# Performance work log

Measured on AMD Instinct MI355X. Metric: run time of the kernel, lower is better.

The kernel has to match this reference:

```python
import jax, jax.numpy as jnp
import numpy as np
from jax import lax

B, C, SD = 2, 64, 512
DW = 2 * C   # DW_Expand=2
FFN = 2 * C  # FFN_Expand=2
D = H = W = 64
K = 3


def _ln3d(x, w, b, eps=1e-6):
    # torch LayerNorm3d: mean/std over channel dim, std is unbiased (ddof=1)
    m = jnp.mean(x, axis=1, keepdims=True)
    s = jnp.std(x, axis=1, keepdims=True, ddof=1)
    return w * ((x - m) / (s + eps)) + b


def _pw(x, w, b):
    # 1x1x1 conv: w [O, I], x [B, I, D, H, W]
    return jnp.einsum('oi,bidhw->bodhw', w, x) + b[None, :, None, None, None]


def setup_inputs() -> dict:
    key = jax.random.key(0)
    ks = jax.random.split(key, 24)
    n = lambda i, shp, sc=1.0: (jax.random.normal(ks[i], shp, jnp.float32) * sc)
    return {
        'inp': n(0, (B, C, D, H, W)),
        'style_vector': n(1, (B, SD)),
        'w1': n(2, (DW, C), 0.1), 'b1': n(3, (DW,), 0.1),
        'mod_w': n(4, (DW, 1, K, K, K), 0.1), 'mod_b': n(5, (DW,), 0.1),
        'style_w': n(6, (DW, SD), 0.05), 'style_b': jnp.ones((DW,), jnp.float32),
        'sca_w': n(7, (DW, DW), 0.1), 'sca_b': n(8, (DW,), 0.1),
        'w3': n(9, (C, DW), 0.1), 'b3': n(10, (C,), 0.1),
        'w4': n(11, (FFN, C), 0.1), 'b4': n(12, (FFN,), 0.1),
        'w5': n(13, (C, FFN), 0.1), 'b5': n(14, (C,), 0.1),
        'ln1_w': jnp.ones((1, C, 1, 1, 1), jnp.float32), 'ln1_b': jnp.zeros((1, C, 1, 1, 1), jnp.float32),
        'ln2_w': jnp.ones((1, C, 1, 1, 1), jnp.float32), 'ln2_b': jnp.zeros((1, C, 1, 1, 1), jnp.float32),
        'beta': n(15, (1, C, 1, 1, 1), 0.1), 'gamma': n(16, (1, C, 1, 1, 1), 0.1),
    }


def _mod_dwconv(x, style, mod_w, mod_b, style_w, style_b):
    # StyleGAN-style per-sample modulated DEPTHWISE 3x3x3 conv.
    # For a depthwise conv, modulating weight per (sample, channel) and
    # demodulating is equivalent to one shared depthwise conv followed by a
    # per-(sample, channel) output scale s*demod.
    s = style @ style_w.T + style_b                      # [B, DW]
    k2 = jnp.sum(mod_w * mod_w, axis=(1, 2, 3, 4))       # [DW]
    demod = lax.rsqrt(k2[None, :] * (s * s) + 1e-8)      # [B, DW]
    y = lax.conv_general_dilated(
        x, mod_w, window_strides=(1, 1, 1), padding=((1, 1), (1, 1), (1, 1)),
        dimension_numbers=('NCDHW', 'OIDHW', 'NCDHW'), feature_group_count=DW)
    return y * (s * demod)[:, :, None, None, None] + mod_b[None, :, None, None, None]


def reference(inp, style_vector, w1, b1, mod_w, mod_b, style_w, style_b,
              sca_w, sca_b, w3, b3, w4, b4, w5, b5,
              ln1_w, ln1_b, ln2_w, ln2_b, beta, gamma):
    x = _ln3d(inp, ln1_w, ln1_b)
    x = _pw(x, w1, b1)
    x = _mod_dwconv(x, style_vector, mod_w, mod_b, style_w, style_b)
    x = jax.nn.gelu(x, approximate=False)
    pooled = jnp.mean(x, axis=(2, 3, 4), keepdims=True)          # [B, DW, 1,1,1]
    gate = jnp.einsum('oi,bicde->bocde', sca_w, pooled) + sca_b[None, :, None, None, None]
    x = x * gate
    x = _pw(x, w3, b3)
    y = inp + x * beta
    x = _pw(_ln3d(y, ln2_w, ln2_b), w4, b4)
    x = jax.nn.gelu(x, approximate=False)
    x = _pw(x, w5, b5)
    return y + x * gamma
```

## Files before the change

### kernel.cpp

```cpp
#include <hip/hip_runtime.h>
#include <hip/hip_bf16.h>

typedef __hip_bfloat16 bf16;
typedef short  sv4 __attribute__((ext_vector_type(4)));
typedef short  sv8 __attribute__((ext_vector_type(8)));
typedef float  f32x4 __attribute__((ext_vector_type(4)));
typedef float  fv2  __attribute__((ext_vector_type(2)));
typedef unsigned int uv4 __attribute__((ext_vector_type(4)));

#define CH      64
#define DWC     128
#define SDIM    512
#define SPATIAL (64*64*64)
#define NB      2
#define NVOX    (NB*SPATIAL)

#define ROWS      65
#define PLANE_CH  (64*ROWS)
#define BG_CH     (64*PLANE_CH)
#define HPAD_CHUNKS ((size_t)32*BG_CH + 16)
#define HPAD_BYTES  (HPAD_CHUNKS*16)

#define OFF_SMOD   0
#define OFF_POOLED 256
#define OFF_PB1    512
#define OFF_PB4    768
#define OFF_PB35   1024
#define OFF_MODWT  1536
#define OFF_U16    5120
#define U16_W1F 0
#define U16_W3F 8192
#define U16_W4F 24576
#define U16_W5F 32768

#define A_BYTES ((size_t)NB * DWC * SPATIAL * 2)

__device__ __forceinline__ float b2f(short u) {
    return __uint_as_float(((unsigned)(unsigned short)u) << 16);
}
__device__ __forceinline__ short f2bs(float f) {
    __hip_bfloat16 h = __float2bfloat16(f);
    return __builtin_bit_cast(short, h);
}
__device__ __forceinline__ float gelu_f(float x) {
    float x2 = x * x;
    float z  = x * fmaf(x2, 0.07135481627f, 1.5957691216f);
    float e  = exp2f(-1.4426950409f * z);
    return x * __builtin_amdgcn_rcpf(1.f + e);
}

__global__ void prep_kernel(const float* __restrict__ style,
                            const float* __restrict__ w1, const float* __restrict__ b1,
                            const float* __restrict__ mod_w,
                            const float* __restrict__ style_w, const float* __restrict__ style_b,
                            const float* __restrict__ b3,
                            const float* __restrict__ w4, const float* __restrict__ b4,
                            const float* __restrict__ w5, const float* __restrict__ b5,
                            const float* __restrict__ ln1w, const float* __restrict__ ln1b,
                            const float* __restrict__ ln2w, const float* __restrict__ ln2b,
                            const float* __restrict__ beta, const float* __restrict__ gamma,
                            float* __restrict__ wsf, sv8* __restrict__ h) {
    int t = threadIdx.x;
    int B = blockIdx.x;
    short* w16 = (short*)(wsf + OFF_U16);

    if (B == 0) {
        if (t < 16) {
            const sv8 zz = {0,0,0,0,0,0,0,0};
            h[(size_t)32*BG_CH + t] = zz;
        }
        if (t < DWC) {
            float bb1 = b1[t], bb4 = b4[t];
            for (int c = 0; c < CH; ++c) {
                bb1 = fmaf(w1[t*CH + c], ln1b[c], bb1);
                bb4 = fmaf(w4[t*CH + c], ln2b[c], bb4);
            }
            wsf[OFF_PB1 + t] = bb1;
            wsf[OFF_PB4 + t] = bb4;
        }
        if (t < CH) {
            wsf[OFF_PB35 + 4*t + 0] = b3[t];
            wsf[OFF_PB35 + 4*t + 1] = beta[t];
            wsf[OFF_PB35 + 4*t + 2] = gamma[t];
            wsf[OFF_PB35 + 4*t + 3] = b5[t];
        }
        for (int idx = t; idx < 27*DWC; idx += 256) {
            int k = idx >> 7, c = idx & 127;
            wsf[OFF_MODWT + idx] = mod_w[c*27 + k];
        }
    }
    {
        int o   = B*32 + (t >> 3);
        int sub = t & 7;
        int b = o >> 7, ch = o & 127;
        const float4* s4 = (const float4*)(style + b*SDIM) + sub*16;
        const float4* wv = (const float4*)(style_w + ch*SDIM) + sub*16;
        float s0=0.f, s1=0.f, s2=0.f, s3=0.f;
        #pragma unroll
        for (int i = 0; i < 16; ++i) {
            float4 a_ = s4[i], b_ = wv[i];
            s0 = fmaf(a_.x, b_.x, s0); s1 = fmaf(a_.y, b_.y, s1);
            s2 = fmaf(a_.z, b_.z, s2); s3 = fmaf(a_.w, b_.w, s3);
        }
        float ps = (s0 + s1) + (s2 + s3);
        ps += __shfl_xor(ps, 1); ps += __shfl_xor(ps, 2); ps += __shfl_xor(ps, 4);
        if (sub == 0) {
            float s = style_b[ch] + ps;
            float k2 = 0.f;
            for (int j = 0; j < 27; ++j) { float w = mod_w[ch*27 + j]; k2 = fmaf(w, w, k2); }
            wsf[OFF_SMOD + o]   = s * rsqrtf(fmaf(k2, s*s, 1e-8f));
            wsf[OFF_POOLED + o] = 0.f;
        }
    }
    for (int idx = B*1024 + t; idx < B*1024 + 1024; idx += 256) {
        int m = idx >> 6, k = idx & 63;
        int dst = (((k >> 3)*DWC + m) << 3) + (k & 7);
        w16[U16_W1F + dst] = f2bs(w1[idx] * ln1w[k]);
        w16[U16_W4F + dst] = f2bs(w4[idx] * ln2w[k]);
    }
    for (int idx = B*1024 + t; idx < B*1024 + 1024; idx += 256) {
        int m = idx >> 7, k = idx & 127;
        w16[U16_W5F + (((k >> 3)*CH + m) << 3) + (k & 7)] = f2bs(w5[idx]);
    }
}

__global__ __launch_bounds__(256) void lnpw1_kernel(const float* __restrict__ inp,
                                                    const float* __restrict__ wsf,
                                                    sv8* __restrict__ h) {
    __shared__ sv8  w1s[1024];
    __shared__ short ht[4*2176];
    int tid  = threadIdx.x;
    int blk  = blockIdx.x;
    int wid  = tid >> 6;
    int lane = tid & 63;
    int col  = lane & 15, grp = lane >> 4;
    int b    = blk >> 12;
    int row  = blk & 4095;
    int vx   = (row << 6) + (wid << 4) + col;

    const float* b1p = wsf + OFF_PB1;
    short* hw = ht + wid*2176;

    const float* xp = inp + (size_t)b * CH * SPATIAL + vx;
    float xv[16];
    #pragma unroll
    for (int e = 0; e < 16; ++e) {
        int k = ((e >> 3) << 5) + (grp << 3) + (e & 7);
        xv[e] = xp[(size_t)k * SPATIAL];
    }
    {
        const sv8* src = (const sv8*)((const short*)(wsf + OFF_U16) + U16_W1F);
        #pragma unroll
        for (int i = 0; i < 4; ++i) w1s[i*256 + tid] = src[i*256 + tid];
    }
    __syncthreads();

    float sum = 0.f, ssq = 0.f;
    #pragma unroll
    for (int e = 0; e < 16; ++e) { sum += xv[e]; ssq = fmaf(xv[e], xv[e], ssq); }
    sum += __shfl_xor(sum, 16); sum += __shfl_xor(sum, 32);
    ssq += __shfl_xor(ssq, 16); ssq += __shfl_xor(ssq, 32);
    float m   = sum * (1.f/64.f);
    float var = fmaxf((ssq - 64.f*m*m) * (1.f/63.f), 0.f);
    float inv = 1.f / (sqrtf(var) + 1e-6f);

    sv8 xb0, xb1;
    #pragma unroll
    for (int i = 0; i < 8; ++i) {
        xb0[i] = f2bs((xv[i]     - m) * inv);
        xb1[i] = f2bs((xv[8 + i] - m) * inv);
    }

    f32x4 acc[8] = {};
    #pragma unroll
    for (int mt = 0; mt < 8; ++mt) {
        acc[mt] = __builtin_amdgcn_mfma_f32_16x16x32_bf16(w1s[(grp    )*DWC + mt*16 + col], xb0, acc[mt], 0, 0, 0);
        acc[mt] = __builtin_amdgcn_mfma_f32_16x16x32_bf16(w1s[(grp + 4)*DWC + mt*16 + col], xb1, acc[mt], 0, 0, 0);
    }

    #pragma unroll
    for (int mt = 0; mt < 8; ++mt) {
        sv4 p;
        #pragma unroll
        for (int r = 0; r < 4; ++r) {
            int f = mt*16 + 4*grp + r;
            p[r] = f2bs(acc[mt][r] + b1p[f]);
        }
        *(sv4*)(hw + col*136 + mt*16 + 4*grp) = p;
    }
    #pragma unroll
    for (int gq = 0; gq < 4; ++gq) {
        int g = gq*4 + grp;
        sv8 vrow = *(const sv8*)(hw + col*136 + g*8);
        size_t base = (size_t)(b*16 + g) * BG_CH + row*ROWS;
        h[base + 1 + (wid << 4) + col] = vrow;
        if (wid == 0 && col == 0) {
            const sv8 zz = {0,0,0,0,0,0,0,0};
            h[base] = zz;
        }
    }
}

__global__ __launch_bounds__(256) void conv_kernel(const sv8* __restrict__ h,
                                                   const float* __restrict__ mod_b,
                                                   const float* __restrict__ wsf,
                                                   sv8* __restrict__ a,
                                                   float* __restrict__ pooled) {
    __shared__ float part[4][8];
    int tid = threadIdx.x;
    int w   = tid & 63;
    int dq  = tid >> 6;
    int hy  = blockIdx.x & 63;
    int bg  = blockIdx.x >> 6;
    int g   = bg & 15;
    int b   = bg >> 4;

    const sv8* hP  = h + (size_t)bg * BG_CH;
    sv8*      adst = a + (size_t)bg * SPATIAL;
    const float* mwt = wsf + OFF_MODWT + g*8;
    const float* smp = wsf + OFF_SMOD + b*DWC + g*8;
    const float* mbp = mod_b + g*8;

    bool r0ok = (hy > 0), r2ok = (hy < 63);
    int d0 = dq << 4;

    fv2 an[4] = {}, am[4] = {}, ao[4] = {};
    fv2 psum[4] = {};

    #pragma unroll 1
    for (int i = 0; i < 18; ++i) {
        int dd = d0 - 1 + i;
        fv2 f[9][4];
        if ((unsigned)dd < 64u) {
            const sv8* p = hP + dd*PLANE_CH + hy*ROWS + 1 + w;
            sv8 cv[9];
            const sv8 zz = {0,0,0,0,0,0,0,0};
            if (r0ok) { cv[0] = p[-ROWS-1]; cv[1] = p[-ROWS]; cv[2] = p[-ROWS+1]; }
            else      { cv[0] = zz; cv[1] = zz; cv[2] = zz; }
            cv[3] = p[-1]; cv[4] = p[0]; cv[5] = p[1];
            if (r2ok) { cv[6] = p[ROWS-1]; cv[7] = p[ROWS]; cv[8] = p[ROWS+1]; }
            else      { cv[6] = zz; cv[7] = zz; cv[8] = zz; }
            #pragma unroll
            for (int r = 0; r < 9; ++r) {
                uv4 u = __builtin_bit_cast(uv4, cv[r]);
                #pragma unroll
                for (int c4 = 0; c4 < 4; ++c4) {
                    fv2 fr;
                    fr.x = __uint_as_float(u[c4] << 16);
                    fr.y = __uint_as_float(u[c4] & 0xFFFF0000u);
                    f[r][c4] = fr;
                }
            }
        } else {
            #pragma unroll
            for (int r = 0; r < 9; ++r)
                #pragma unroll
                for (int c4 = 0; c4 < 4; ++c4) f[r][c4] = (fv2)(0.f);
        }

        if (i >= 2) {
            #pragma unroll
            for (int r = 0; r < 9; ++r) {
                const fv2* wr = (const fv2*)(mwt + (18 + r)*DWC);
                #pragma unroll
                for (int c4 = 0; c4 < 4; ++c4) ao[c4] = wr[c4]*f[r][c4] + ao[c4];
            }
            int o = d0 + i - 2;
            sv8 ov;
            #pragma unroll
            for (int c4 = 0; c4 < 4; ++c4) {
                float v0 = gelu_f(fmaf(ao[c4].x, smp[2*c4],     mbp[2*c4]));
                float v1 = gelu_f(fmaf(ao[c4].y, smp[2*c4 + 1], mbp[2*c4 + 1]));
                psum[c4].x += v0; psum[c4].y += v1;
                ov[2*c4]     = f2bs(v0);
                ov[2*c4 + 1] = f2bs(v1);
            }
            adst[o*4096 + hy*64 + w] = ov;
        }
        if (i >= 1 && i <= 16) {
            #pragma unroll
            for (int r = 0; r < 9; ++r) {
                const fv2* wr = (const fv2*)(mwt + (9 + r)*DWC);
                #pragma unroll
                for (int c4 = 0; c4 < 4; ++c4) am[c4] = wr[c4]*f[r][c4] + am[c4];
            }
        }
        if (i <= 15) {
            #pragma unroll
            for (int c4 = 0; c4 < 4; ++c4) an[c4] = (fv2)(0.f);
            #pragma unroll
            for (int r = 0; r < 9; ++r) {
                const fv2* wr = (const fv2*)(mwt + r*DWC);
                #pragma unroll
                for (int c4 = 0; c4 < 4; ++c4) an[c4] = wr[c4]*f[r][c4] + an[c4];
            }
        }
        #pragma unroll
        for (int c4 = 0; c4 < 4; ++c4) { ao[c4] = am[c4]; am[c4] = an[c4]; }
    }

    #pragma unroll
    for (int c = 0; c < 8; ++c) {
        float s = (c & 1) ? psum[c >> 1].y : psum[c >> 1].x;
        #pragma unroll
        for (int off = 32; off > 0; off >>= 1) s += __shfl_xor(s, off);
        if ((tid & 63) == 0) part[dq][c] = s;
    }
    __syncthreads();
    if (tid < 8)
        atomicAdd(&pooled[b*DWC + g*8 + tid],
                  part[0][tid] + part[1][tid] + part[2][tid] + part[3][tid]);
}

__global__ void gate_kernel(const float* __restrict__ sca_w,
                            const float* __restrict__ sca_b,
                            const float* __restrict__ w3,
                            float* __restrict__ wsf) {
    __shared__ float gsh[256];
    int t = threadIdx.x;
    int b = t >> 7, o = t & 127;
    const float invS = 1.f / (float)SPATIAL;
    float gval = sca_b[o];
    for (int i = 0; i < DWC; ++i)
        gval = fmaf(sca_w[o*DWC + i], wsf[OFF_POOLED + b*DWC + i] * invS, gval);
    gsh[t] = gval;
    __syncthreads();
    int e = blockIdx.x * 256 + t;
    int bb = e >> 10, kf = (e >> 6) & 15, m = e & 63;
    sv8 frag;
    #pragma unroll
    for (int i = 0; i < 8; ++i) {
        int k = kf*8 + i;
        frag[i] = f2bs(w3[m*DWC + k] * gsh[bb*DWC + k]);
    }
    sv8* w3f = (sv8*)((short*)(wsf + OFF_U16) + U16_W3F);
    w3f[e] = frag;
}

__global__ __launch_bounds__(256) void tail_kernel(const float* __restrict__ inp,
                                                   const sv8* __restrict__ a,
                                                   const float* __restrict__ wsf,
                                                   float* __restrict__ out) {
    __shared__ sv8  w3s[1024];
    __shared__ short yt[4][2176];
    int tid  = threadIdx.x;
    int wid  = tid >> 6;
    int lane = tid & 63;
    int col  = lane & 15, grp = lane >> 4;
    int blk  = blockIdx.x;
    int b    = blk >> 12;
    int vx   = ((blk & 4095) << 6) + (wid << 4) + col;

    const short* w16 = (const short*)(wsf + OFF_U16);
    const sv8* W4 = (const sv8*)(w16 + U16_W4F);
    const sv8* W5 = (const sv8*)(w16 + U16_W5F);
    const float*  b4p  = wsf + OFF_PB4;
    const float4* pb35 = (const float4*)(wsf + OFF_PB35);
    short* yw = &yt[wid][0];

    sv8 bq[4];
    #pragma unroll
    for (int ks = 0; ks < 4; ++ks)
        bq[ks] = a[(size_t)(b*16 + ks*4 + grp) * SPATIAL + vx];
    float xin[16];
    #pragma unroll
    for (int j = 0; j < 16; ++j) {
        int c = (j >> 2)*16 + 4*grp + (j & 3);
        xin[j] = inp[((size_t)(b*CH + c)) * SPATIAL + vx];
    }
    {
        const sv8* src = (const sv8*)(w16 + U16_W3F) + (size_t)b * 1024;
        #pragma unroll
        for (int i = 0; i < 4; ++i) w3s[i*256 + tid] = src[i*256 + tid];
    }
    __syncthreads();

    f32x4 acc3[4] = {};
    #pragma unroll
    for (int mt = 0; mt < 4; ++mt)
        #pragma unroll
        for (int ks = 0; ks < 4; ++ks)
            acc3[mt] = __builtin_amdgcn_mfma_f32_16x16x32_bf16(
                w3s[(ks*4 + grp)*64 + mt*16 + col], bq[ks], acc3[mt], 0, 0, 0);

    float y[16];
    float sum = 0.f, ssq = 0.f;
    #pragma unroll
    for (int mt = 0; mt < 4; ++mt)
        #pragma unroll
        for (int r = 0; r < 4; ++r) {
            int c = mt*16 + 4*grp + r;
            float4 pb = pb35[c];
            float tt = acc3[mt][r] + pb.x;
            float yv = fmaf(tt, pb.y, xin[mt*4 + r]);
            y[mt*4 + r] = yv; sum += yv; ssq = fmaf(yv, yv, ssq);
        }
    sum += __shfl_xor(sum, 16); sum += __shfl_xor(sum, 32);
    ssq += __shfl_xor(ssq, 16); ssq += __shfl_xor(ssq, 32);
    float m2   = sum * (1.f/64.f);
    float var2 = fmaxf((ssq - 64.f*m2*m2) * (1.f/63.f), 0.f);
    float inv2 = 1.f / (sqrtf(var2) + 1e-6f);

    #pragma unroll
    for (int mt = 0; mt < 4; ++mt) {
        sv4 p;
        #pragma unroll
        for (int r = 0; r < 4; ++r)
            p[r] = f2bs((y[mt*4 + r] - m2) * inv2);
        *(sv4*)(yw + col*136 + mt*16 + 4*grp) = p;
    }
    sv8 by0 = *(const sv8*)(yw + col*136 + grp*8);
    sv8 by1 = *(const sv8*)(yw + col*136 + grp*8 + 32);

    f32x4 acc4[8] = {};
    #pragma unroll
    for (int mt = 0; mt < 8; ++mt) {
        acc4[mt] = __builtin_amdgcn_mfma_f32_16x16x32_bf16(W4[(grp    )*DWC + mt*16 + col], by0, acc4[mt], 0, 0, 0);
        acc4[mt] = __builtin_amdgcn_mfma_f32_16x16x32_bf16(W4[(grp + 4)*DWC + mt*16 + col], by1, acc4[mt], 0, 0, 0);
    }

    #pragma unroll
    for (int mt = 0; mt < 8; ++mt) {
        sv4 p;
        #pragma unroll
        for (int r = 0; r < 4; ++r) {
            int f = mt*16 + 4*grp + r;
            p[r] = f2bs(gelu_f(acc4[mt][r] + b4p[f]));
        }
        *(sv4*)(yw + col*136 + mt*16 + 4*grp) = p;
    }
    sv8 bg[4];
    #pragma unroll
    for (int ks = 0; ks < 4; ++ks)
        bg[ks] = *(const sv8*)(yw + col*136 + grp*8 + ks*32);

    f32x4 acc5[4] = {};
    #pragma unroll
    for (int mt = 0; mt < 4; ++mt)
        #pragma unroll
        for (int ks = 0; ks < 4; ++ks)
            acc5[mt] = __builtin_amdgcn_mfma_f32_16x16x32_bf16(
                W5[(ks*4 + grp)*64 + mt*16 + col], bg[ks], acc5[mt], 0, 0, 0);

    #pragma unroll
    for (int mt = 0; mt < 4; ++mt)
        #pragma unroll
        for (int r = 0; r < 4; ++r) {
            int c = mt*16 + 4*grp + r;
            float4 pb = pb35[c];
            float o = fmaf(acc5[mt][r] + pb.w, pb.z, y[mt*4 + r]);
            out[((size_t)(b*CH + c)) * SPATIAL + vx] = o;
        }
}

extern "C" void kernel_launch(void* const* d_in, const int* in_sizes, int n_in,
                              void* d_out, int out_size, void* d_ws, size_t ws_size,
                              hipStream_t stream) {
    const float* inp     = (const float*)d_in[0];
    const float* style   = (const float*)d_in[1];
    const float* w1      = (const float*)d_in[2];
    const float* b1      = (const float*)d_in[3];
    const float* mod_w   = (const float*)d_in[4];
    const float* mod_b   = (const float*)d_in[5];
    const float* style_w = (const float*)d_in[6];
    const float* style_b = (const float*)d_in[7];
    const float* sca_w   = (const float*)d_in[8];
    const float* sca_b   = (const float*)d_in[9];
    const float* w3      = (const float*)d_in[10];
    const float* b3      = (const float*)d_in[11];
    const float* w4      = (const float*)d_in[12];
    const float* b4      = (const float*)d_in[13];
    const float* w5      = (const float*)d_in[14];
    const float* b5      = (const float*)d_in[15];
    const float* ln1w    = (const float*)d_in[16];
    const float* ln1b    = (const float*)d_in[17];
    const float* ln2w    = (const float*)d_in[18];
    const float* ln2b    = (const float*)d_in[19];
    const float* beta    = (const float*)d_in[20];
    const float* gamma   = (const float*)d_in[21];

    sv8*   h   = (sv8*)d_ws;
    sv8*   a   = (sv8*)((char*)d_ws + HPAD_BYTES);
    float* wsf = (float*)((char*)d_ws + HPAD_BYTES + A_BYTES);
    float* out = (float*)d_out;

    prep_kernel<<<8, 256, 0, stream>>>(style, w1, b1, mod_w, style_w, style_b,
                                       b3, w4, b4, w5, b5,
                                       ln1w, ln1b, ln2w, ln2b, beta, gamma, wsf, h);
    lnpw1_kernel<<<8192, 256, 0, stream>>>(inp, wsf, h);
    conv_kernel<<<2048, 256, 0, stream>>>(h, mod_b, wsf, a, wsf + OFF_POOLED);
    gate_kernel<<<8, 256, 0, stream>>>(sca_w, sca_b, w3, wsf);
    tail_kernel<<<8192, 256, 0, stream>>>(inp, a, wsf, out);
}
```

Baseline: 330.5 us.

## Double-buffer depthwise conv plane loads and vectorize gate matvec

Restructures the depthwise conv loop to load the next D-plane into a second register buffer while computing on the current one. Each plane now issues all three depth-tap accumulations in one pass with fused bf16 unpacking. The loop is unrolled by two, so loads overlap with FMAs. The gate kernel stages the pooled means in shared memory and reads sca_w with float4 loads. This raises register pressure from holding two 9-vector plane buffers, which could cut occupancy.

```diff
diff --git a/kernel.cpp b/kernel.cpp
--- a/kernel.cpp
+++ b/kernel.cpp
@@ -223,49 +223,44 @@
 
     bool r0ok = (hy > 0), r2ok = (hy < 63);
     int d0 = dq << 4;
+    const sv8 zz = {0,0,0,0,0,0,0,0};
 
     fv2 an[4] = {}, am[4] = {}, ao[4] = {};
     fv2 psum[4] = {};
 
-    #pragma unroll 1
-    for (int i = 0; i < 18; ++i) {
-        int dd = d0 - 1 + i;
-        fv2 f[9][4];
+    auto LOADP = [&](int dd, sv8* cv) {
         if ((unsigned)dd < 64u) {
             const sv8* p = hP + dd*PLANE_CH + hy*ROWS + 1 + w;
-            sv8 cv[9];
-            const sv8 zz = {0,0,0,0,0,0,0,0};
             if (r0ok) { cv[0] = p[-ROWS-1]; cv[1] = p[-ROWS]; cv[2] = p[-ROWS+1]; }
             else      { cv[0] = zz; cv[1] = zz; cv[2] = zz; }
             cv[3] = p[-1]; cv[4] = p[0]; cv[5] = p[1];
             if (r2ok) { cv[6] = p[ROWS-1]; cv[7] = p[ROWS]; cv[8] = p[ROWS+1]; }
             else      { cv[6] = zz; cv[7] = zz; cv[8] = zz; }
-            #pragma unroll
-            for (int r = 0; r < 9; ++r) {
-                uv4 u = __builtin_bit_cast(uv4, cv[r]);
-                #pragma unroll
-                for (int c4 = 0; c4 < 4; ++c4) {
-                    fv2 fr;
-                    fr.x = __uint_as_float(u[c4] << 16);
-                    fr.y = __uint_as_float(u[c4] & 0xFFFF0000u);
-                    f[r][c4] = fr;
-                }
-            }
         } else {
             #pragma unroll
-            for (int r = 0; r < 9; ++r)
-                #pragma unroll
-                for (int c4 = 0; c4 < 4; ++c4) f[r][c4] = (fv2)(0.f);
-        }
-
-        if (i >= 2) {
+            for (int r = 0; r < 9; ++r) cv[r] = zz;
+        }
+    };
+
+    auto COMPUTE = [&](int pi, const sv8* cv) {
+        #pragma unroll
+        for (int r = 0; r < 9; ++r) {
+            uv4 u = __builtin_bit_cast(uv4, cv[r]);
+            const fv2* w2 = (const fv2*)(mwt + (18 + r)*DWC);
+            const fv2* w1_ = (const fv2*)(mwt + (9 + r)*DWC);
+            const fv2* w0 = (const fv2*)(mwt + r*DWC);
             #pragma unroll
-            for (int r = 0; r < 9; ++r) {
-                const fv2* wr = (const fv2*)(mwt + (18 + r)*DWC);
-                #pragma unroll
-                for (int c4 = 0; c4 < 4; ++c4) ao[c4] = wr[c4]*f[r][c4] + ao[c4];
+            for (int c4 = 0; c4 < 4; ++c4) {
+                fv2 fr;
+                fr.x = __uint_as_float(u[c4] << 16);
+                fr.y = __uint_as_float(u[c4] & 0xFFFF0000u);
+                ao[c4] = w2[c4]*fr + ao[c4];
+                am[c4] = w1_[c4]*fr + am[c4];
+                an[c4] = w0[c4]*fr + an[c4];
             }
-            int o = d0 + i - 2;
+        }
+        if (pi >= 2) {
+            int o = d0 + pi - 2;
             sv8 ov;
             #pragma unroll
             for (int c4 = 0; c4 < 4; ++c4) {
@@ -277,26 +272,20 @@
             }
             adst[o*4096 + hy*64 + w] = ov;
         }
-        if (i >= 1 && i <= 16) {
-            #pragma unroll
-            for (int r = 0; r < 9; ++r) {
-                const fv2* wr = (const fv2*)(mwt + (9 + r)*DWC);
-                #pragma unroll
-                for (int c4 = 0; c4 < 4; ++c4) am[c4] = wr[c4]*f[r][c4] + am[c4];
-            }
-        }
-        if (i <= 15) {
-            #pragma unroll
-            for (int c4 = 0; c4 < 4; ++c4) an[c4] = (fv2)(0.f);
-            #pragma unroll
-            for (int r = 0; r < 9; ++r) {
-                const fv2* wr = (const fv2*)(mwt + r*DWC);
-                #pragma unroll
-                for (int c4 = 0; c4 < 4; ++c4) an[c4] = wr[c4]*f[r][c4] + an[c4];
-            }
-        }
-        #pragma unroll
-        for (int c4 = 0; c4 < 4; ++c4) { ao[c4] = am[c4]; am[c4] = an[c4]; }
+        #pragma unroll
+        for (int c4 = 0; c4 < 4; ++c4) {
+            ao[c4] = am[c4]; am[c4] = an[c4]; an[c4] = (fv2)(0.f);
+        }
+    };
+
+    sv8 cvA[9], cvB[9];
+    LOADP(d0 - 1, cvA);
+    #pragma unroll 1
+    for (int pi = 0; pi < 18; pi += 2) {
+        LOADP(d0 + pi, cvB);
+        COMPUTE(pi, cvA);
+        if (pi < 16) LOADP(d0 + pi + 1, cvA);
+        COMPUTE(pi + 1, cvB);
     }
 
     #pragma unroll
@@ -317,12 +306,23 @@
                             const float* __restrict__ w3,
                             float* __restrict__ wsf) {
     __shared__ float gsh[256];
+    __shared__ float psh[256];
     int t = threadIdx.x;
+    const float invS = 1.f / (float)SPATIAL;
+    psh[t] = wsf[OFF_POOLED + t] * invS;
+    __syncthreads();
     int b = t >> 7, o = t & 127;
-    const float invS = 1.f / (float)SPATIAL;
+    const float4* wv = (const float4*)(sca_w + o*DWC);
+    const float*  pp = psh + b*DWC;
     float gval = sca_b[o];
-    for (int i = 0; i < DWC; ++i)
-        gval = fmaf(sca_w[o*DWC + i], wsf[OFF_POOLED + b*DWC + i] * invS, gval);
+    #pragma unroll
+    for (int i = 0; i < 32; ++i) {
+        float4 wq = wv[i];
+        gval = fmaf(wq.x, pp[4*i+0], gval);
+        gval = fmaf(wq.y, pp[4*i+1], gval);
+        gval = fmaf(wq.z, pp[4*i+2], gval);
+        gval = fmaf(wq.w, pp[4*i+3], gval);
+    }
     gsh[t] = gval;
     __syncthreads();
     int e = blockIdx.x * 256 + t;
```

Result: slower. 377.6 us (+14.3%).
